# Performance work log

Hardware: AMD Instinct MI355X
Metric: run time of the kernel (lower is better)

The kernel has to match this reference:

```python
import jax, jax.numpy as jnp
import numpy as np

BITS = 4
GROUP = 128
IN_F = 4096
OUT_F = 4096
MAXQ = (1 << BITS) - 1  # 15
TOKENS = 8192


def setup_inputs() -> dict:
    key = jax.random.key(0)
    k1, k2, k3, k4, k5 = jax.random.split(key, 5)
    x = jax.random.normal(k1, (TOKENS, IN_F), dtype=jnp.float32)
    # packed 4-bit weights: 8 values per int32 word along the input dim
    qweight = jax.random.randint(k2, (IN_F // 32 * BITS, OUT_F), 0, 2147483647, dtype=jnp.int32)
    # packed 4-bit zero points: 8 values per int32 word along the output dim
    qzeros = jax.random.randint(k3, (IN_F // GROUP, OUT_F // 32 * BITS), 0, 2147483647, dtype=jnp.int32)
    scales = jax.random.uniform(k4, (IN_F // GROUP, OUT_F), dtype=jnp.float32, minval=0.001, maxval=0.02)
    bias = jax.random.normal(k5, (OUT_F,), dtype=jnp.float32)
    g_idx = (jnp.arange(IN_F) // GROUP).astype(jnp.int32)
    return {"x": x, "qweight": qweight, "qzeros": qzeros, "scales": scales, "bias": bias, "g_idx": g_idx}


def _dequantize(qweight, qzeros, scales, g_idx):
    # shift amounts for the 32//BITS = 8 nibbles packed per int32 word
    shifts = jnp.arange(0, 32, BITS, dtype=jnp.int32)
    # unpack weights: [IN//32*BITS, 8, OUT] -> [IN, OUT], values in [0, MAXQ]
    w = (qweight[:, None, :] >> shifts[None, :, None]) & MAXQ
    w = w.reshape(IN_F, OUT_F)
    # unpack zero points: [G, OUT//32*BITS, 8] -> [G, OUT]
    z = (qzeros[:, :, None] >> shifts[None, None, :]) & MAXQ
    z = z.reshape(scales.shape[0], OUT_F)
    # per-group dequant: W = s[g] * (w - z[g])  (tritonv2 dequant, no +1 on zeros)
    gi = g_idx.astype(jnp.int32)
    W = scales[gi] * (w.astype(scales.dtype) - z[gi].astype(scales.dtype))
    return W  # [IN, OUT]


def reference(x, qweight, qzeros, scales, bias, g_idx):
    W = _dequantize(qweight, qzeros, scales, g_idx)
    out = x @ W + bias  # [TOKENS, OUT]
    return out
```

## Files before the change

kernel.cpp:

```cpp
#include <hip/hip_runtime.h>
#include <hip/hip_bf16.h>
#include <stdint.h>

#define TOKENS 8192
#define IN_F   4096
#define OUT_F  4096
#define GROUP  128

typedef __attribute__((ext_vector_type(4))) int   i32x4;
typedef __attribute__((ext_vector_type(4))) float f32x4;

__global__ __launch_bounds__(256) void k_quant_x(const float* __restrict__ x,
                                                 int8_t* __restrict__ xq,
                                                 float* __restrict__ xs) {
  const int row = blockIdx.x;
  const int t = threadIdx.x;
  const float4* xr = (const float4*)(x + (size_t)row * IN_F) + t * 4;
  float f[16];
  *(float4*)&f[0] = xr[0];
  *(float4*)&f[4] = xr[1];
  *(float4*)&f[8] = xr[2];
  *(float4*)&f[12] = xr[3];
  float am = 0.f;
#pragma unroll
  for (int j = 0; j < 16; ++j) am = fmaxf(am, fabsf(f[j]));
#pragma unroll
  for (int off = 32; off; off >>= 1) am = fmaxf(am, __shfl_xor(am, off));
  __shared__ float red[4];
  if ((t & 63) == 0) red[t >> 6] = am;
  __syncthreads();
  am = fmaxf(fmaxf(red[0], red[1]), fmaxf(red[2], red[3]));
  am = fmaxf(am, 1e-8f);
  const float inv = 127.f / am;
  if (t == 0) xs[row] = am / 127.f;
  union {
    i32x4 v;
    int8_t c[16];
  } u;
#pragma unroll
  for (int j = 0; j < 16; ++j) u.c[j] = (int8_t)__float2int_rn(f[j] * inv);
  ((i32x4*)(xq + (size_t)row * IN_F))[t] = u.v;
}

__global__ __launch_bounds__(256) void k_requant_w8(
    const int* __restrict__ qweight, const int* __restrict__ qzeros,
    const float* __restrict__ scales, int8_t* __restrict__ wq,
    float* __restrict__ sw) {
  __shared__ float smax[16][17];
  const int n0 = blockIdx.x * 16;
  const int col = threadIdx.x & 15;
  const int seg = threadIdx.x >> 4;
  const int n = n0 + col;

  int zloc[2];
  float sloc[2];
  float m = 0.f;
#pragma unroll
  for (int i = 0; i < 2; ++i) {
    const int g = seg * 2 + i;
    const unsigned zw =
        ((const unsigned*)qzeros)[(size_t)g * (OUT_F / 8) + (n >> 3)];
    const int z = (int)((zw >> ((n & 7) * 4)) & 15u);
    const float s = scales[(size_t)g * OUT_F + n];
    zloc[i] = z;
    sloc[i] = s;
    m = fmaxf(m, s * (float)(z > 15 - z ? z : 15 - z));
  }
  smax[col][seg] = m;
  __syncthreads();
  float Sw = 0.f;
#pragma unroll
  for (int ss = 0; ss < 16; ++ss) Sw = fmaxf(Sw, smax[col][ss]);
  Sw /= 127.f;
  if (seg == 0) sw[n] = Sw;
  const float inv = 1.f / Sw;

#pragma unroll
  for (int i = 0; i < 2; ++i) {
    const int g = seg * 2 + i;
    const int z = zloc[i];
    const float f = sloc[i] * inv;
#pragma unroll
    for (int kw = 0; kw < 16; ++kw) {
      const unsigned w =
          ((const unsigned*)qweight)[(size_t)(g * 16 + kw) * OUT_F + n];
      unsigned lo = 0, hi = 0;
#pragma unroll
      for (int j = 0; j < 8; ++j) {
        const int q = (int)((w >> (4 * j)) & 15u);
        const int v = __float2int_rn(f * (float)(q - z));
        const unsigned b = (unsigned)(v & 255);
        if (j < 4)
          lo |= b << (8 * j);
        else
          hi |= b << (8 * (j - 4));
      }
      uint2 pk = {lo, hi};
      *(uint2*)(wq + (size_t)n * IN_F + (size_t)(g * 16 + kw) * 8) = pk;
    }
  }
}

__device__ inline void gload_lds16(const void* g, void* l) {
  __builtin_amdgcn_global_load_lds(
      (const __attribute__((address_space(1))) void*)g,
      (__attribute__((address_space(3))) void*)l, 16, 0, 0);
}

#define STAGE_T(buf, tile)                                                    \
  do {                                                                        \
    _Pragma("unroll") for (int i_ = 0; i_ < 4; ++i_) {                        \
      gload_lds16(Ag + goffS[i_] + (size_t)((tile) & 31) * 128,               \
                  smem + (buf)*32768 + ldsS[i_]);                             \
    }                                                                         \
    _Pragma("unroll") for (int i_ = 0; i_ < 4; ++i_) {                        \
      gload_lds16(Bg + goffS[i_] + (size_t)((tile) & 31) * 128,               \
                  smem + (buf)*32768 + 16384 + ldsS[i_]);                     \
    }                                                                         \
  } while (0)

#define PHASE(bufc, T)                                                        \
  do {                                                                        \
    _Pragma("unroll") for (int nf_ = 0; nf_ < 4; ++nf_) {                     \
      const char* p_ =                                                        \
          smem + (bufc)*32768 + 16384 + (wc * 64 + nf_ * 16 + fr) * 128;      \
      bF[nf_][0] = *(const i32x4*)(p_ + csw0);                                \
      bF[nf_][1] = *(const i32x4*)(p_ + csw1);                                \
    }                                                                         \
    _Pragma("unroll") for (int mf_ = 0; mf_ < 4; ++mf_) {                     \
      const char* p_ = smem + (bufc)*32768 + (wr * 64 + mf_ * 16 + fr) * 128; \
      aF[mf_][0] = *(const i32x4*)(p_ + csw0);                                \
      aF[mf_][1] = *(const i32x4*)(p_ + csw1);                                \
    }                                                                         \
    asm volatile("s_waitcnt lgkmcnt(0)" ::: "memory");                        \
    __builtin_amdgcn_sched_barrier(0);                                        \
    __builtin_amdgcn_s_barrier();          \
    STAGE_T(bufc, (T) + 2);                   \
    __builtin_amdgcn_s_setprio(1);                                            \
    _Pragma("unroll") for (int nf_ = 0; nf_ < 4; ++nf_)                       \
        _Pragma("unroll") for (int mf_ = 0; mf_ < 4; ++mf_) {                 \
      iacc[mf_][nf_] = __builtin_amdgcn_mfma_i32_16x16x64_i8(                 \
          aF[mf_][0], bF[nf_][0], iacc[mf_][nf_], 0, 0, 0);                   \
    }                                                                         \
    _Pragma("unroll") for (int nf_ = 0; nf_ < 4; ++nf_)                       \
        _Pragma("unroll") for (int mf_ = 0; mf_ < 4; ++mf_) {                 \
      iacc[mf_][nf_] = __builtin_amdgcn_mfma_i32_16x16x64_i8(                 \
          aF[mf_][1], bF[nf_][1], iacc[mf_][nf_], 0, 0, 0);                   \
    }                                                                         \
    __builtin_amdgcn_s_setprio(0);                                            \
    __builtin_amdgcn_sched_barrier(0);                                        \
    asm volatile("s_waitcnt vmcnt(8)" ::: "memory");                          \
    __builtin_amdgcn_s_barrier();                                             \
  } while (0)

__global__ __launch_bounds__(256, 2) void k_gemm_i8(
    const int8_t* __restrict__ xq,
    const int8_t* __restrict__ wq,
    const float* __restrict__ sw,
    const float* __restrict__ xs,
    const float* __restrict__ bias,
    float* __restrict__ out) {
  extern __shared__ __align__(16) char smem[];

  const int bidx = blockIdx.x;
  const int xcd = bidx & 7;
  const int slot = bidx >> 3;
  const int bm = slot >> 2;
  const int bn = xcd * 4 + (slot & 3);
  const int m0 = bm * 128;
  const int n0 = bn * 128;

  const int t = threadIdx.x;
  const int lane = t & 63;
  const int wid = t >> 6;
  const int wr = wid >> 1;
  const int wc = wid & 1;
  const int fr = lane & 15;
  const int hq = lane >> 4;

  const int csw0 = (hq ^ (fr & 7)) * 16;
  const int csw1 = ((hq ^ 4) ^ (fr & 7)) * 16;

  int goffS[4], ldsS[4];
#pragma unroll
  for (int i = 0; i < 4; ++i) {
    const int srow = wid * 32 + i * 8 + (lane >> 3);
    const int sch = (lane & 7) ^ (srow & 7);
    goffS[i] = srow * IN_F + sch * 16;
    ldsS[i] = (wid * 4 + i) * 1024;
  }

  const char* Ag = (const char*)(xq + (size_t)m0 * IN_F);
  const char* Bg = (const char*)(wq + (size_t)n0 * IN_F);

  i32x4 iacc[4][4];
#pragma unroll
  for (int i = 0; i < 4; ++i)
#pragma unroll
    for (int j = 0; j < 4; ++j) iacc[i][j] = (i32x4){0, 0, 0, 0};

  i32x4 aF[4][2];
  i32x4 bF[4][2];

  STAGE_T(0, 0);
  STAGE_T(1, 1);
  asm volatile("s_waitcnt vmcnt(8) lgkmcnt(0)" ::: "memory");
  __builtin_amdgcn_s_barrier();

#pragma unroll 1
  for (int it = 0; it < 16; ++it) {
    const int T = 2 * it;
    PHASE(0, T);
    PHASE(1, T + 1);
  }

  float swv[4], bv[4];
#pragma unroll
  for (int nf = 0; nf < 4; ++nf) {
    const int n = n0 + wc * 64 + nf * 16 + fr;
    swv[nf] = sw[n];
    bv[nf] = bias[n];
  }
#pragma unroll
  for (int mf = 0; mf < 4; ++mf) {
#pragma unroll
    for (int r = 0; r < 4; ++r) {
      const int m = m0 + wr * 64 + mf * 16 + hq * 4 + r;
      const float xsv = xs[m];
      float* o = out + (size_t)m * OUT_F + n0;
#pragma unroll
      for (int nf = 0; nf < 4; ++nf) {
        o[wc * 64 + nf * 16 + fr] =
            xsv * swv[nf] * (float)iacc[mf][nf][r] + bv[nf];
      }
    }
  }
}

extern "C" void kernel_launch(void* const* d_in, const int* in_sizes, int n_in,
                              void* d_out, int out_size, void* d_ws,
                              size_t ws_size, hipStream_t stream) {
  const float* x = (const float*)d_in[0];
  const int* qweight = (const int*)d_in[1];
  const int* qzeros = (const int*)d_in[2];
  const float* scales = (const float*)d_in[3];
  const float* bias = (const float*)d_in[4];
  float* out = (float*)d_out;

  int8_t* xq = (int8_t*)d_ws;
  int8_t* wq = xq + (size_t)TOKENS * IN_F;
  float* xs = (float*)(wq + (size_t)OUT_F * IN_F);
  float* sw = xs + TOKENS;

  (void)hipFuncSetAttribute(reinterpret_cast<const void*>(&k_gemm_i8),
                            hipFuncAttributeMaxDynamicSharedMemorySize, 65536);

  k_quant_x<<<TOKENS, 256, 0, stream>>>(x, xq, xs);
  k_requant_w8<<<OUT_F / 16, 256, 0, stream>>>(qweight, qzeros, scales, wq, sw);
  k_gemm_i8<<<(TOKENS / 128) * (OUT_F / 128), 256, 65536, stream>>>(
      xq, wq, sw, xs, bias, out);
}
```

Before: 183.4 us.

## Enlarge int8 GEMM block tile to 256x256 with 8 waves

Doubles the GEMM block tile in both M and N to 256x256, uses 512 threads arranged as 2x4 waves each computing a 128x64 sub-tile, and doubles the LDS double-buffer to 128KB. This raises the arithmetic intensity per staged byte and halves global/L2 traffic per MFMA, and the staging index math and XCD block mapping are rewritten to match. The cost is one block per CU from the LDS footprint, heavier register pressure (32 accumulators), and a grid of only 512 blocks, which risks tail imbalance and less latency hiding.

```diff
diff --git a/kernel.cpp b/kernel.cpp
--- a/kernel.cpp
+++ b/kernel.cpp
@@ -109,43 +109,38 @@
 
 #define STAGE_T(buf, tile)                                                    \
   do {                                                                        \
-    _Pragma("unroll") for (int i_ = 0; i_ < 4; ++i_) {                        \
-      gload_lds16(Ag + goffS[i_] + (size_t)((tile) & 31) * 128,               \
-                  smem + (buf)*32768 + ldsS[i_]);                             \
-    }                                                                         \
-    _Pragma("unroll") for (int i_ = 0; i_ < 4; ++i_) {                        \
-      gload_lds16(Bg + goffS[i_] + (size_t)((tile) & 31) * 128,               \
-                  smem + (buf)*32768 + 16384 + ldsS[i_]);                     \
+    _Pragma("unroll") for (int r_ = 0; r_ < 4; ++r_) {                        \
+      gload_lds16(Ag + goff[r_] + (size_t)((tile) & 31) * 128,                \
+                  smem + (buf)*65536 + ldsoff[r_]);                           \
+    }                                                                         \
+    _Pragma("unroll") for (int r_ = 0; r_ < 4; ++r_) {                        \
+      gload_lds16(Bg + goff[r_] + (size_t)((tile) & 31) * 128,                \
+                  smem + (buf)*65536 + 32768 + ldsoff[r_]);                   \
     }                                                                         \
   } while (0)
 
 #define PHASE(bufc, T)                                                        \
   do {                                                                        \
+    const char* aB_ = smem + (bufc)*65536 + (wr * 128 + fr) * 128;            \
+    const char* bB_ = smem + (bufc)*65536 + 32768 + (wc * 64 + fr) * 128;     \
+    _Pragma("unroll") for (int mf_ = 0; mf_ < 8; ++mf_) {                     \
+      aF[mf_][0] = *(const i32x4*)(aB_ + mf_ * 2048 + csw0);                  \
+      aF[mf_][1] = *(const i32x4*)(aB_ + mf_ * 2048 + csw1);                  \
+    }                                                                         \
     _Pragma("unroll") for (int nf_ = 0; nf_ < 4; ++nf_) {                     \
-      const char* p_ =                                                        \
-          smem + (bufc)*32768 + 16384 + (wc * 64 + nf_ * 16 + fr) * 128;      \
-      bF[nf_][0] = *(const i32x4*)(p_ + csw0);                                \
-      bF[nf_][1] = *(const i32x4*)(p_ + csw1);                                \
-    }                                                                         \
-    _Pragma("unroll") for (int mf_ = 0; mf_ < 4; ++mf_) {                     \
-      const char* p_ = smem + (bufc)*32768 + (wr * 64 + mf_ * 16 + fr) * 128; \
-      aF[mf_][0] = *(const i32x4*)(p_ + csw0);                                \
-      aF[mf_][1] = *(const i32x4*)(p_ + csw1);                                \
+      bF[nf_][0] = *(const i32x4*)(bB_ + nf_ * 2048 + csw0);                  \
+      bF[nf_][1] = *(const i32x4*)(bB_ + nf_ * 2048 + csw1);                  \
     }                                                                         \
     asm volatile("s_waitcnt lgkmcnt(0)" ::: "memory");                        \
     __builtin_amdgcn_sched_barrier(0);                                        \
     __builtin_amdgcn_s_barrier();          \
     STAGE_T(bufc, (T) + 2);                   \
     __builtin_amdgcn_s_setprio(1);                                            \
-    _Pragma("unroll") for (int nf_ = 0; nf_ < 4; ++nf_)                       \
-        _Pragma("unroll") for (int mf_ = 0; mf_ < 4; ++mf_) {                 \
+    _Pragma("unroll") for (int kk_ = 0; kk_ < 2; ++kk_)                       \
+        _Pragma("unroll") for (int nf_ = 0; nf_ < 4; ++nf_)                   \
+            _Pragma("unroll") for (int mf_ = 0; mf_ < 8; ++mf_) {             \
       iacc[mf_][nf_] = __builtin_amdgcn_mfma_i32_16x16x64_i8(                 \
-          aF[mf_][0], bF[nf_][0], iacc[mf_][nf_], 0, 0, 0);                   \
-    }                                                                         \
-    _Pragma("unroll") for (int nf_ = 0; nf_ < 4; ++nf_)                       \
-        _Pragma("unroll") for (int mf_ = 0; mf_ < 4; ++mf_) {                 \
-      iacc[mf_][nf_] = __builtin_amdgcn_mfma_i32_16x16x64_i8(                 \
-          aF[mf_][1], bF[nf_][1], iacc[mf_][nf_], 0, 0, 0);                   \
+          aF[mf_][kk_], bF[nf_][kk_], iacc[mf_][nf_], 0, 0, 0);               \
     }                                                                         \
     __builtin_amdgcn_s_setprio(0);                                            \
     __builtin_amdgcn_sched_barrier(0);                                        \
@@ -153,7 +148,7 @@
     __builtin_amdgcn_s_barrier();                                             \
   } while (0)
 
-__global__ __launch_bounds__(256, 2) void k_gemm_i8(
+__global__ __launch_bounds__(512, 2) void k_gemm_i8(
     const int8_t* __restrict__ xq,
     const int8_t* __restrict__ wq,
     const float* __restrict__ sw,
@@ -165,41 +160,42 @@
   const int bidx = blockIdx.x;
   const int xcd = bidx & 7;
   const int slot = bidx >> 3;
-  const int bm = slot >> 2;
-  const int bn = xcd * 4 + (slot & 3);
-  const int m0 = bm * 128;
-  const int n0 = bn * 128;
+  const int bm = slot >> 1;
+  const int bn = xcd * 2 + (slot & 1);
+  const int m0 = bm * 256;
+  const int n0 = bn * 256;
 
   const int t = threadIdx.x;
   const int lane = t & 63;
   const int wid = t >> 6;
-  const int wr = wid >> 1;
-  const int wc = wid & 1;
+  const int wr = wid >> 2;
+  const int wc = wid & 3;
   const int fr = lane & 15;
   const int hq = lane >> 4;
 
   const int csw0 = (hq ^ (fr & 7)) * 16;
   const int csw1 = ((hq ^ 4) ^ (fr & 7)) * 16;
 
-  int goffS[4], ldsS[4];
-#pragma unroll
-  for (int i = 0; i < 4; ++i) {
-    const int srow = wid * 32 + i * 8 + (lane >> 3);
-    const int sch = (lane & 7) ^ (srow & 7);
-    goffS[i] = srow * IN_F + sch * 16;
-    ldsS[i] = (wid * 4 + i) * 1024;
+  int goff[4], ldsoff[4];
+#pragma unroll
+  for (int r = 0; r < 4; ++r) {
+    const int c = r * 512 + t;
+    const int srow = c >> 3;
+    const int sch = (c & 7) ^ (srow & 7);
+    goff[r] = srow * IN_F + sch * 16;
+    ldsoff[r] = (r * 512 + wid * 64) * 16;
   }
 
   const char* Ag = (const char*)(xq + (size_t)m0 * IN_F);
   const char* Bg = (const char*)(wq + (size_t)n0 * IN_F);
 
-  i32x4 iacc[4][4];
-#pragma unroll
-  for (int i = 0; i < 4; ++i)
+  i32x4 iacc[8][4];
+#pragma unroll
+  for (int i = 0; i < 8; ++i)
 #pragma unroll
     for (int j = 0; j < 4; ++j) iacc[i][j] = (i32x4){0, 0, 0, 0};
 
-  i32x4 aF[4][2];
+  i32x4 aF[8][2];
   i32x4 bF[4][2];
 
   STAGE_T(0, 0);
@@ -222,10 +218,10 @@
     bv[nf] = bias[n];
   }
 #pragma unroll
-  for (int mf = 0; mf < 4; ++mf) {
+  for (int mf = 0; mf < 8; ++mf) {
 #pragma unroll
     for (int r = 0; r < 4; ++r) {
-      const int m = m0 + wr * 64 + mf * 16 + hq * 4 + r;
+      const int m = m0 + wr * 128 + mf * 16 + hq * 4 + r;
       const float xsv = xs[m];
       float* o = out + (size_t)m * OUT_F + n0;
 #pragma unroll
@@ -253,10 +249,10 @@
   float* sw = xs + TOKENS;
 
   (void)hipFuncSetAttribute(reinterpret_cast<const void*>(&k_gemm_i8),
-                            hipFuncAttributeMaxDynamicSharedMemorySize, 65536);
+                            hipFuncAttributeMaxDynamicSharedMemorySize, 131072);
 
   k_quant_x<<<TOKENS, 256, 0, stream>>>(x, xq, xs);
   k_requant_w8<<<OUT_F / 16, 256, 0, stream>>>(qweight, qzeros, scales, wq, sw);
-  k_gemm_i8<<<(TOKENS / 128) * (OUT_F / 128), 256, 65536, stream>>>(
+  k_gemm_i8<<<(TOKENS / 256) * (OUT_F / 256), 512, 131072, stream>>>(
       xq, wq, sw, xs, bias, out);
 }
```

Result: slower. 187.9 us (+2.5%).
